# Performance work log

Hardware: AMD Instinct MI355X
Metric: run time of the kernel (lower is better)

The kernel has to match this reference:

```python
import jax, jax.numpy as jnp
import numpy as np

EMBED, ACT, DETER, STOCH, HID = 1536, 10, 2048, 64, 1024
T, B = 64, 256
LN_EPS = 1e-3


def _ln(x, s, b):
    mu = jnp.mean(x, axis=-1, keepdims=True)
    var = jnp.mean(jnp.square(x - mu), axis=-1, keepdims=True)
    return (x - mu) * jax.lax.rsqrt(var + LN_EPS) * s + b


def setup_inputs() -> dict:
    key = jax.random.key(0)
    ks = jax.random.split(key, 20)
    g = lambda k, shp, fan: jax.random.normal(k, shp, jnp.float32) * (1.0 / np.sqrt(fan))
    inp = {
        "embeds": jax.random.normal(ks[0], (T, B, EMBED), jnp.float32),
        "actions": jax.random.normal(ks[1], (T, B, ACT), jnp.float32),
        "h_t": jnp.zeros((B, DETER), jnp.float32),
        "z_t": jnp.zeros((B, STOCH), jnp.float32),
        "noise": jax.random.normal(ks[2], (T, B, STOCH), jnp.float32),
        # DeterNext
        "z_mlp_w": g(ks[3], (HID // 2, STOCH), STOCH),
        "z_mlp_b": jnp.zeros((HID // 2,), jnp.float32),
        "a_mlp_w": g(ks[4], (HID // 2, ACT), ACT),  # bias=False
        "ln_za_s": jnp.ones((HID,), jnp.float32),
        "ln_za_b": jnp.zeros((HID,), jnp.float32),
        # GRUCell (torch layout: [3*deter, in])
        "gru_wih": g(ks[5], (3 * DETER, HID), HID),
        "gru_whh": g(ks[6], (3 * DETER, DETER), DETER),
        "gru_bih": jnp.zeros((3 * DETER,), jnp.float32),
        "gru_bhh": jnp.zeros((3 * DETER,), jnp.float32),
        # PosteriorNext
        "post_h_w": g(ks[7], (HID, DETER), DETER),
        "post_h_b": jnp.zeros((HID,), jnp.float32),
        "post_e_w": g(ks[8], (HID, EMBED), EMBED),
        "post_e_b": jnp.zeros((HID,), jnp.float32),
        "ln_post_s": jnp.ones((HID,), jnp.float32),
        "ln_post_b": jnp.zeros((HID,), jnp.float32),
        "post_w": g(ks[9], (2 * STOCH, HID), HID),
        "post_b": jnp.zeros((2 * STOCH,), jnp.float32),
        # PriorNext
        "prior_h_w": g(ks[10], (HID, DETER), DETER),
        "prior_h_b": jnp.zeros((HID,), jnp.float32),
        "ln_prior_s": jnp.ones((HID,), jnp.float32),
        "ln_prior_b": jnp.zeros((HID,), jnp.float32),
        "prior_w": g(ks[11], (2 * STOCH, HID), HID),
        "prior_b": jnp.zeros((2 * STOCH,), jnp.float32),
    }
    return inp


def _rssm_forward(embeds, actions, h0, z0, noise,
                  z_mlp_w, z_mlp_b, a_mlp_w, ln_za_s, ln_za_b,
                  gru_wih, gru_whh, gru_bih, gru_bhh,
                  post_h_w, post_h_b, post_e_w, post_e_b, ln_post_s, ln_post_b,
                  post_w, post_b,
                  prior_h_w, prior_h_b, ln_prior_s, ln_prior_b, prior_w, prior_b):
    def step(carry, xs):
        h, z = carry
        e, a, n = xs
        # DeterNext: concat(z_mlp(z), a_mlp(a)) -> LN -> ELU
        x = jnp.concatenate([z @ z_mlp_w.T + z_mlp_b, a @ a_mlp_w.T], axis=-1)
        za = jax.nn.elu(_ln(x, ln_za_s, ln_za_b))
        # GRUCell
        gi = za @ gru_wih.T + gru_bih
        gh = h @ gru_whh.T + gru_bhh
        ir, iu, ic = jnp.split(gi, 3, axis=-1)
        hr, hu, hc = jnp.split(gh, 3, axis=-1)
        r = jax.nn.sigmoid(ir + hr)
        u = jax.nn.sigmoid(iu + hu)
        c = jnp.tanh(ic + r * hc)
        h1 = (1.0 - u) * c + u * h
        # PosteriorNext
        p = jax.nn.elu(_ln(h1 @ post_h_w.T + post_h_b + e @ post_e_w.T + post_e_b,
                           ln_post_s, ln_post_b))
        post = p @ post_w.T + post_b  # [B, 2*stoch]
        mean, sraw = jnp.split(post, 2, axis=-1)
        std = 2.0 * jax.nn.sigmoid(sraw) + 0.1
        z1 = mean + std * n  # rsample with externally-supplied noise
        return (h1, z1), (post, h1, z1)

    (_, _), (posts, states_h, post_z_samples) = jax.lax.scan(
        step, (h0, z0), (embeds, actions, noise))
    # batch prior over all timesteps
    pr = jax.nn.elu(_ln(states_h @ prior_h_w.T + prior_h_b, ln_prior_s, ln_prior_b))
    priors = pr @ prior_w.T + prior_b  # [T, B, 2*stoch]
    features = jnp.concatenate([states_h, post_z_samples], axis=-1)  # [T,B,deter+stoch]
    return priors, posts, post_z_samples, features


def reference(embeds, actions, h_t, z_t, noise,
              z_mlp_w, z_mlp_b, a_mlp_w, ln_za_s, ln_za_b,
              gru_wih, gru_whh, gru_bih, gru_bhh,
              post_h_w, post_h_b, post_e_w, post_e_b, ln_post_s, ln_post_b,
              post_w, post_b,
              prior_h_w, prior_h_b, ln_prior_s, ln_prior_b, prior_w, prior_b):
    return _rssm_forward(embeds, actions, h_t, z_t, noise,
                         z_mlp_w, z_mlp_b, a_mlp_w, ln_za_s, ln_za_b,
                         gru_wih, gru_whh, gru_bih, gru_bhh,
                         post_h_w, post_h_b, post_e_w, post_e_b, ln_post_s, ln_post_b,
                         post_w, post_b,
                         prior_h_w, prior_h_b, ln_prior_s, ln_prior_b, prior_w, prior_b)
```

## Files before the change

### kernel.cpp

```cpp
#include <hip/hip_runtime.h>

#define LN_EPS 1e-3f

typedef short s8v __attribute__((ext_vector_type(8)));
typedef float f4v __attribute__((ext_vector_type(4)));
typedef unsigned short u16;

#define MFMA16 __builtin_amdgcn_mfma_f32_16x16x32_bf16

__device__ __forceinline__ u16 f2bf(float f) {
  unsigned int x = __float_as_uint(f);
  x += 0x7fffu + ((x >> 16) & 1u);
  return (u16)(x >> 16);
}
__device__ __forceinline__ float bf2f(u16 u) {
  return __uint_as_float(((unsigned int)u) << 16);
}

__device__ __forceinline__ void glds16(const u16* g, void* l) {
  __builtin_amdgcn_global_load_lds(
      (const __attribute__((address_space(1))) void*)g,
      (__attribute__((address_space(3))) void*)l, 16, 0, 0);
}

#define RAW_BAR() do { __builtin_amdgcn_s_barrier(); __builtin_amdgcn_sched_barrier(0); } while (0)

__global__ void k_cvt(const float* __restrict__ src, u16* __restrict__ dst, int n) {
  int i = blockIdx.x * blockDim.x + threadIdx.x;
  int stride = gridDim.x * blockDim.x;
  for (; i < n; i += stride) dst[i] = f2bf(src[i]);
}

__global__ void k_packgru(const float* __restrict__ wih,
                          const float* __restrict__ whh, u16* __restrict__ wt) {
  int u = blockIdx.x * 256 + threadIdx.x;
  int nt = u / 73728;
  int r1 = u % 73728;
  int s = r1 / 1536;
  int r2 = r1 % 1536;
  int sub = r2 / 512;
  int r3 = r2 % 512;
  int ch = r3 / 64;
  int row = r3 % 64;
  int j = nt * 64 + row;
  int kbase = s * 64 + ch * 8;
  s8v v;
#pragma unroll
  for (int e = 0; e < 8; ++e) {
    int kk = kbase + e;
    float x;
    if (sub == 0) {
      x = kk < 1024 ? wih[(size_t)j * 1024 + kk] : whh[(size_t)j * 2048 + kk - 1024];
    } else if (sub == 1) {
// ... 56 lines not shown
  if (tid < 64) zsh[tid] = zsrc[b * 64 + tid];
  if (tid < 10) ash[tid] = act[b * 10 + tid];
  __syncthreads();
  float x[4];
#pragma unroll
  for (int i = 0; i < 2; ++i) {
    int c = tid + i * 256;
    const float4* wp = (const float4*)(zw + c * 64);
    float a = zb[c];
#pragma unroll
    for (int k = 0; k < 16; ++k) {
      float4 v = wp[k];
      a += zsh[k * 4] * v.x + zsh[k * 4 + 1] * v.y + zsh[k * 4 + 2] * v.z +
           zsh[k * 4 + 3] * v.w;
    }
    x[i] = a;
  }
#pragma unroll
  for (int i = 2; i < 4; ++i) {
    int c2 = tid + (i - 2) * 256;
    const float* wp = aw + c2 * 10;
    float a = 0.f;
#pragma unroll
    for (int k = 0; k < 10; ++k) a += ash[k] * wp[k];
    x[i] = a;
  }
  float s = x[0] + x[1] + x[2] + x[3];
#pragma unroll
  for (int o = 1; o < 64; o <<= 1) s += __shfl_xor(s, o);
  if ((tid & 63) == 0) wred[tid >> 6] = s;
  __syncthreads();
  float mu = (wred[0] + wred[1] + wred[2] + wred[3]) * (1.f / 1024.f);
  float q = 0.f;
#pragma unroll
  for (int i = 0; i < 4; ++i) {
    float d = x[i] - mu;
    q += d * d;
  }
#pragma unroll
  for (int o = 1; o < 64; o <<= 1) q += __shfl_xor(q, o);
  if ((tid & 63) == 0) wred[4 + (tid >> 6)] = q;
  __syncthreads();
  float rs = rsqrtf((wred[4] + wred[5] + wred[6] + wred[7]) * (1.f / 1024.f) + LN_EPS);
  int cols[4] = {tid, tid + 256, 512 + tid, 768 + tid};
#pragma unroll
  for (int i = 0; i < 4; ++i) {
    int c = cols[i];
    float y = (x[i] - mu) * rs * lns[c] + lnb[c];
    y = y > 0.f ? y : expm1f(y);
    za[(size_t)b * 1024 + c] = f2bf(y);
  }
}

__global__ __launch_bounds__(512) void k_gru(
    const u16* __restrict__ za, const u16* __restrict__ hcat_r,
    const u16* __restrict__ wt, const float* __restrict__ bih,
    const float* __restrict__ bhh, const float* __restrict__ hf_r,
    float* __restrict__ hf_w, u16* __restrict__ hcat_w,
    float* __restrict__ feat, int t) {
  const int hw = blockIdx.x;
  const int logical = (hw & 7) * 16 + (hw >> 3);
  const int mg = logical & 3;
  const int nt = logical >> 2;
  const int m0 = mg * 64;
  const int tid = threadIdx.x;
  const int lane = tid & 63;
  const int w = tid >> 6;
  const int lr = lane & 15, lk = lane >> 4;
  const int mh = w & 1, cq = w >> 1;

  __shared__ __align__(16) char bufs[3][32768];

  const int arow = w * 8 + (lane >> 3);
  const int acol8 = ((lane & 7) ^ (arow & 7)) * 8;
  const u16* aZ = za + (size_t)(m0 + arow) * 1024 + acol8;
  const u16* aH = hcat_r + (size_t)(m0 + arow) * 2048 + acol8;
  const u16* wtNt = wt + (size_t)nt * 48 * 12288;

  f4v accr0 = (f4v)(0.f), accr1 = (f4v)(0.f);
  f4v accu0 = (f4v)(0.f), accu1 = (f4v)(0.f);
  f4v acci0 = (f4v)(0.f), acci1 = (f4v)(0.f);
  f4v acch0 = (f4v)(0.f), acch1 = (f4v)(0.f);

#define G_STAGE(S) { \
    char* base = &bufs[(S) % 3][0]; \
    const u16* ap = ((S) < 16) ? (aZ + (S) * 64) : (aH + ((S) - 16) * 64); \
    glds16(ap, base + w * 1024); \
    const u16* bsrc = wtNt + (size_t)(S) * 12288; \
    _Pragma("unroll") for (int jj = 0; jj < 3; ++jj) { \
      int c = w + jj * 8; \
      glds16(bsrc + c * 512 + lane * 8, base + 8192 + c * 1024); \
    } }

#define G_COMP(S, X0, X1) { \
    char* base = &bufs[(S) % 3][0]; \
    _Pragma("unroll") for (int kk = 0; kk < 2; ++kk) { \
      int ch = kk * 4 + lk; \
      int r0 = mh * 32 + lr, r1 = mh * 32 + 16 + lr; \
      s8v a0 = *(const s8v*)(base + r0 * 128 + ((ch ^ (r0 & 7)) << 4)); \
      s8v a1 = *(const s8v*)(base + r1 * 128 + ((ch ^ (r1 & 7)) << 4)); \
      int boff = 8192 + ch * 1024 + ((cq * 16 + lr) << 4); \
      s8v br = *(const s8v*)(base + boff); \
      s8v bu = *(const s8v*)(base + boff + 8192); \
      s8v bx = *(const s8v*)(base + boff + 16384); \
      accr0 = MFMA16(a0, br, accr0, 0, 0, 0); \
      accr1 = MFMA16(a1, br, accr1, 0, 0, 0); \
      accu0 = MFMA16(a0, bu, accu0, 0, 0, 0); \
      accu1 = MFMA16(a1, bu, accu1, 0, 0, 0); \
      X0 = MFMA16(a0, bx, X0, 0, 0, 0); \
      X1 = MFMA16(a1, bx, X1, 0, 0, 0); \
    } }

  G_STAGE(0)
  G_STAGE(1)
  for (int s = 0; s < 48; ++s) {
    if (s + 2 < 48) { G_STAGE(s + 2) }
    if (s < 46) asm volatile("s_waitcnt vmcnt(8)" ::: "memory");
    else if (s == 46) asm volatile("s_waitcnt vmcnt(4)" ::: "memory");
    else asm volatile("s_waitcnt vmcnt(0)" ::: "memory");
    RAW_BAR();
    if (s < 16) { G_COMP(s, acci0, acci1) }
    else { G_COMP(s, acch0, acch1) }
    RAW_BAR();
  }
#undef G_STAGE
#undef G_COMP

  const int col = nt * 64 + cq * 16 + lr;
  const float b_r = bih[col] + bhh[col];
  const float b_u = bih[2048 + col] + bhh[2048 + col];
  const float b_ci = bih[4096 + col];
  const float b_ch = bhh[4096 + col];
#define G_EPI(AR, AU, AI, AH, MO) \
  _Pragma("unroll") for (int r = 0; r < 4; ++r) { \
    int grow = m0 + mh * 32 + (MO) + lk * 4 + r; \
    float vr = AR[r] + b_r; \
    float vu = AU[r] + b_u; \
    float ic = AI[r] + b_ci; \
    float hc = AH[r] + b_ch; \
    float rg = 1.f / (1.f + expf(-vr)); \
    float ug = 1.f / (1.f + expf(-vu)); \
    float c = tanhf(ic + rg * hc); \
    float hold = hf_r[(size_t)grow * 2048 + col]; \
    float h1 = (1.f - ug) * c + ug * hold; \
    hf_w[(size_t)grow * 2048 + col] = h1; \
    hcat_w[(size_t)grow * 2048 + col] = f2bf(h1); \
    feat[(size_t)(t * 256 + grow) * 2112 + col] = h1; \
  }
  G_EPI(accr0, accu0, acci0, acch0, 0)
  G_EPI(accr1, accu1, acci1, acch1, 16)
#undef G_EPI
}

__global__ __launch_bounds__(256) void k_post(
    const u16* __restrict__ hcat, const u16* __restrict__ wp,
    const float* __restrict__ bias, const u16* __restrict__ epart_t,
    float* __restrict__ xbuf) {
  const int hw = blockIdx.x;
  const int logical = (hw & 7) * 16 + (hw >> 3);
  const int mg = logical & 7, nt = logical >> 3;
  const int m0 = mg * 32;
  const int tid = threadIdx.x;
  const int lane = tid & 63;
  const int w = tid >> 6;
  const int lr = lane & 15, lk = lane >> 4;

  __shared__ __align__(16) char smem[2][12288];

  const int arow = 8 * w + (lane >> 3);
  const int acol8 = ((lane & 7) ^ (arow & 7)) * 8;
  const u16* aSrc = hcat + (size_t)(m0 + arow) * 2048 + acol8;
  const u16* wpNt = wp + (size_t)nt * 32 * 4096;

  f4v acc[2];
  acc[0] = (f4v)(0.f);
  acc[1] = (f4v)(0.f);

#define K2_STAGE(BB, S) { \
    char* base = &smem[BB][0]; \
    glds16(aSrc + (S) * 64, base + w * 1024); \
    const u16* bsrc = wpNt + (size_t)(S) * 4096; \
    _Pragma("unroll") for (int i = 0; i < 2; ++i) { \
      int cf = w + i * 4; \
      glds16(bsrc + (cf * 64 + lane) * 8, base + 4096 + cf * 1024); \
    } }

#define K2_COMP(BB) { \
    char* base = &smem[BB][0]; \
    _Pragma("unroll") for (int kk = 0; kk < 2; ++kk) { \
      int ch = kk * 4 + lk; \
      int r0 = lr, r1 = 16 + lr; \
      s8v a0 = *(const s8v*)(base + r0 * 128 + ((ch ^ (r0 & 7)) * 16)); \
      s8v a1 = *(const s8v*)(base + r1 * 128 + ((ch ^ (r1 & 7)) * 16)); \
      s8v b = *(const s8v*)(base + 4096 + ch * 1024 + (w * 16 + lr) * 16); \
      acc[0] = MFMA16(a0, b, acc[0], 0, 0, 0); \
      acc[1] = MFMA16(a1, b, acc[1], 0, 0, 0); \
    } }

  K2_STAGE(0, 0)
  for (int s = 0; s < 31; ++s) {
    K2_STAGE((s + 1) & 1, s + 1)
    asm volatile("s_waitcnt vmcnt(3)" ::: "memory");
    RAW_BAR();
    K2_COMP(s & 1)
    RAW_BAR();
  }
  {
    asm volatile("s_waitcnt vmcnt(0)" ::: "memory");
    RAW_BAR();
    K2_COMP(1)
  }
#undef K2_STAGE
#undef K2_COMP
  const int col = nt * 64 + w * 16 + lr;
#pragma unroll
  for (int m = 0; m < 2; ++m) {
#pragma unroll
    for (int r = 0; r < 4; ++r) {
      int grow = m0 + m * 16 + lk * 4 + r;
      float v = acc[m][r] + bias[col] + bf2f(epart_t[(size_t)grow * 1024 + col]);
      xbuf[(size_t)grow * 1024 + col] = v;
    }
  }
}

__global__ __launch_bounds__(512) void k_postz(
    const float* __restrict__ xb, const u16* __restrict__ pw,
    const float* __restrict__ lns, const float* __restrict__ lnb,
    const float* __restrict__ pb, float* __restrict__ posts_t,
    const float* __restrict__ noise_t, float* __restrict__ zout,
    float* __restrict__ feat, const u16* __restrict__ zwP,
    const float* __restrict__ zbv, const float* __restrict__ awT,
    const float* __restrict__ act_t, const float* __restrict__ lnzs,
    const float* __restrict__ lnzb, u16* __restrict__ za_out, int t) {
  const int m0 = blockIdx.x * 32;
  const int tid = threadIdx.x;
  const int lane = tid & 63;
  const int w = tid >> 6;
  const int lr = lane & 15, lk = lane >> 4;
  __shared__ __align__(16) u16 As[2][2048];
  __shared__ __align__(16) u16 Bs[2][8192];
  __shared__ float ps[32][132];
  __shared__ float lmu[32], lrsd[32];
  __shared__ __align__(16) u16 zbl[2048];
  __shared__ float ash[320];
  __shared__ __align__(16) char zal[65536];
  __shared__ float zmu[32], zrsd[32];
  __shared__ float psum[16][32], qsum[16][32];

  if (tid < 320) ash[tid] = act_t[m0 * 10 + tid];
  {
    int row = tid >> 4, sg = tid & 15;
    const float4* xp = (const float4*)(xb + (size_t)(m0 + row) * 1024 + sg * 64);
    float s = 0.f, q = 0.f;
#pragma unroll
    for (int i = 0; i < 16; ++i) {
      float4 v = xp[i];
      s += v.x + v.y + v.z + v.w;
      q += v.x * v.x + v.y * v.y + v.z * v.z + v.w * v.w;
    }
#pragma unroll
    for (int o = 1; o < 16; o <<= 1) {
      s += __shfl_xor(s, o);
      q += __shfl_xor(q, o);
    }
    if (sg == 0) {
      float mu = s * (1.f / 1024.f);
      lmu[row] = mu;
      lrsd[row] = rsqrtf(q * (1.f / 1024.f) - mu * mu + LN_EPS);
    }
  }
  __syncthreads();

#define K3_STAGEA(BB, S) if (tid < 256) { \
    int row = tid >> 3, k8 = tid & 7; \
    const float* xp = xb + (size_t)(m0 + row) * 1024 + (S) * 64 + k8 * 8; \
    float mu = lmu[row], rs = lrsd[row]; \
    s8v v; \
    _Pragma("unroll") for (int e = 0; e < 8; ++e) { \
      int c = (S) * 64 + k8 * 8 + e; \
      float y = (xp[e] - mu) * rs * lns[c] + lnb[c]; \
      y = y > 0.f ? y : expm1f(y); \
      v[e] = (short)f2bf(y); \
    } \
    *(s8v*)((char*)&As[BB][0] + row * 128 + ((k8 ^ (row & 7)) * 16)) = v; }

#define K3_STAGEB(BB, S) { \
    const u16* bsrc = pw + (size_t)(S) * 8192; \
    glds16(bsrc + (w * 2) * 512 + lane * 8, (char*)&Bs[BB][0] + w * 2048); \
    glds16(bsrc + (w * 2 + 1) * 512 + lane * 8, (char*)&Bs[BB][0] + w * 2048 + 1024); }

  f4v acc0 = (f4v)(0.f), acc1 = (f4v)(0.f);
  K3_STAGEA(0, 0)
  K3_STAGEB(0, 0)
  int buf = 0;
  for (int s = 0; s < 16; ++s) {
    if (s + 1 < 16) {
      K3_STAGEA(buf ^ 1, s + 1)
      K3_STAGEB(buf ^ 1, s + 1)
      asm volatile("s_waitcnt vmcnt(2) lgkmcnt(0)" ::: "memory");
    } else {
      asm volatile("s_waitcnt vmcnt(0) lgkmcnt(0)" ::: "memory");
    }
    RAW_BAR();
#pragma unroll
    for (int kk = 0; kk < 2; ++kk) {
      int ch = kk * 4 + lk;
      int r0 = lr, r1 = 16 + lr;
      s8v a0 = *(const s8v*)((char*)&As[buf][0] + r0 * 128 + ((ch ^ (r0 & 7)) * 16));
      s8v a1 = *(const s8v*)((char*)&As[buf][0] + r1 * 128 + ((ch ^ (r1 & 7)) * 16));
      s8v b = *(const s8v*)((char*)&Bs[buf][0] + ch * 2048 + (w * 16 + lr) * 16);
      acc0 = MFMA16(a0, b, acc0, 0, 0, 0);
      acc1 = MFMA16(a1, b, acc1, 0, 0, 0);
    }
    __builtin_amdgcn_s_barrier();
    buf ^= 1;
  }
#undef K3_STAGEA
#undef K3_STAGEB

  {
    int colp = w * 16 + lr;
#pragma unroll
    for (int r = 0; r < 4; ++r) {
      int row0 = lk * 4 + r;
      float v0 = acc0[r] + pb[colp];
      posts_t[(size_t)(m0 + row0) * 128 + colp] = v0;
      ps[row0][colp] = v0;
      float v1 = acc1[r] + pb[colp];
      posts_t[(size_t)(m0 + 16 + row0) * 128 + colp] = v1;
      ps[16 + row0][colp] = v1;
    }
  }
  __syncthreads();
#pragma unroll
  for (int q = 0; q < 4; ++q) {
    int e = q * 512 + tid;
    int row = e >> 6, j = e & 63;
    float mean = ps[row][j], sraw = ps[row][64 + j];
    float sd = 2.f / (1.f + expf(-sraw)) + 0.1f;
    float z = mean + sd * noise_t[(m0 + row) * 64 + j];
    zout[(m0 + row) * 64 + j] = z;
    feat[(size_t)(t * 256 + m0 + row) * 2112 + 2048 + j] = z;
    *(u16*)((char*)&zbl[0] + row * 128 + (((j >> 3) ^ (row & 7)) << 4) +
            (j & 7) * 2) = f2bf(z);
  }
  __syncthreads();

  {
    float acc[32];
#pragma unroll
    for (int r = 0; r < 32; ++r) acc[r] = 0.f;
#pragma unroll
    for (int k = 0; k < 10; ++k) {
      float wv = awT[k * 512 + tid];
#pragma unroll
      for (int r = 0; r < 32; ++r) acc[r] += ash[r * 10 + k] * wv;
    }
    int c = 512 + tid;
    int chs = c >> 3, cb = (c & 7) * 2;
#pragma unroll
    for (int r = 0; r < 32; ++r)
      *(u16*)(zal + r * 2048 + ((chs ^ (r & 7)) << 4) + cb) = f2bf(acc[r]);
  }
  for (int c4 = 0; c4 < 4; ++c4) {
    glds16(zwP + c4 * 8192 + (w * 2) * 512 + lane * 8, (char*)&Bs[0][0] + w * 2048);
    glds16(zwP + c4 * 8192 + (w * 2 + 1) * 512 + lane * 8,
           (char*)&Bs[0][0] + w * 2048 + 1024);
    asm volatile("s_waitcnt vmcnt(0)" ::: "memory");
    RAW_BAR();
    f4v z0 = (f4v)(0.f), z1 = (f4v)(0.f);
#pragma unroll
    for (int kk = 0; kk < 2; ++kk) {
      int ch = kk * 4 + lk;
      int r0 = lr, r1 = 16 + lr;
      s8v a0 = *(const s8v*)((char*)&zbl[0] + r0 * 128 + ((ch ^ (r0 & 7)) << 4));
      s8v a1 = *(const s8v*)((char*)&zbl[0] + r1 * 128 + ((ch ^ (r1 & 7)) << 4));
      s8v b = *(const s8v*)((char*)&Bs[0][0] + ch * 2048 + (w * 16 + lr) * 16);
      z0 = MFMA16(a0, b, z0, 0, 0, 0);
      z1 = MFMA16(a1, b, z1, 0, 0, 0);
    }
    int zcol = c4 * 128 + w * 16 + lr;
    int chz = zcol >> 3, cbz = (zcol & 7) * 2;
    float zbias = zbv[zcol];
#pragma unroll
    for (int r = 0; r < 4; ++r) {
      int ra = lk * 4 + r, rb = 16 + lk * 4 + r;
      *(u16*)(zal + ra * 2048 + ((chz ^ (ra & 7)) << 4) + cbz) = f2bf(z0[r] + zbias);
      *(u16*)(zal + rb * 2048 + ((chz ^ (rb & 7)) << 4) + cbz) = f2bf(z1[r] + zbias);
    }
    RAW_BAR();
  }
  __syncthreads();
  {
    int row = tid & 31, g = tid >> 5;
    float s = 0.f, q = 0.f;
#pragma unroll
    for (int jj = 0; jj < 8; ++jj) {
      int chunk = g * 8 + jj;
      s8v v = *(const s8v*)(zal + row * 2048 + ((chunk ^ (row & 7)) << 4));
#pragma unroll
      for (int e = 0; e < 8; ++e) {
        float x = bf2f((u16)v[e]);
        s += x;
        q += x * x;
      }
    }
    psum[g][row] = s;
    qsum[g][row] = q;
    __syncthreads();
    if (tid < 32) {
      float ss = 0.f, qq = 0.f;
#pragma unroll
      for (int gg = 0; gg < 16; ++gg) {
        ss += psum[gg][tid];
        qq += qsum[gg][tid];
      }
      float mu = ss * (1.f / 1024.f);
      zmu[tid] = mu;
      zrsd[tid] = rsqrtf(qq * (1.f / 1024.f) - mu * mu + LN_EPS);
    }
  }
  __syncthreads();
  {
    int row = tid >> 4, g = tid & 15;
    float mu = zmu[row], rs = zrsd[row];
    u16* dst = za_out + (size_t)(m0 + row) * 1024 + g * 64;
#pragma unroll
    for (int jj = 0; jj < 8; ++jj) {
      int chunk = g * 8 + jj;
      s8v v = *(const s8v*)(zal + row * 2048 + ((chunk ^ (row & 7)) << 4));
      s8v o;
#pragma unroll
      for (int e = 0; e < 8; ++e) {
        int c = chunk * 8 + e;
        float y = (bf2f((u16)v[e]) - mu) * rs * lnzs[c] + lnzb[c];
        y = y > 0.f ? y : expm1f(y);
        o[e] = (short)f2bf(y);
      }
      *(s8v*)(dst + jj * 8) = o;
    }
  }
}

template <bool AF32, bool OUTBF16>
__global__ __launch_bounds__(512) void k_gemm8(
    const void* __restrict__ Av, int lda, const u16* __restrict__ Bw, int ldb,
    int nstage, float* __restrict__ Cf, u16* __restrict__ Cb, int ldc,
    const float* __restrict__ bias) {
  const int bx = blockIdx.x, by = blockIdx.y;
  const int tid = threadIdx.x;
  const int m0 = bx * 64;
  const int n0 = by * 128;
  __shared__ __align__(16) u16 As[64][72];
  __shared__ __align__(16) u16 Bs[128][72];
  const int lane = tid & 63;
  const int w = tid >> 6;
  const int wr = w >> 2;
  const int wc = w & 3;
  const int lr = lane & 15;
  const int lk = lane >> 4;

  f4v acc[2][2];
#pragma unroll
  for (int m = 0; m < 2; ++m)
#pragma unroll
    for (int n = 0; n < 2; ++n) acc[m][n] = (f4v)(0.0f);

  for (int s = 0; s < nstage; ++s) {
    const int k0 = s << 6;
    {
      int row = tid >> 3, k8 = (tid & 7) << 3;
      if (AF32) {
        const float* ap = (const float*)Av + (size_t)(m0 + row) * lda + k0 + k8;
        float4 f0 = *(const float4*)ap;
        float4 f1 = *(const float4*)(ap + 4);
        s8v v;
        v[0] = (short)f2bf(f0.x); v[1] = (short)f2bf(f0.y);
        v[2] = (short)f2bf(f0.z); v[3] = (short)f2bf(f0.w);
        v[4] = (short)f2bf(f1.x); v[5] = (short)f2bf(f1.y);
        v[6] = (short)f2bf(f1.z); v[7] = (short)f2bf(f1.w);
        *(s8v*)&As[row][k8] = v;
      } else {
        *(s8v*)&As[row][k8] =
            *(const s8v*)((const u16*)Av + (size_t)(m0 + row) * lda + k0 + k8);
      }
    }
#pragma unroll
    for (int it = 0; it < 2; ++it) {
      int c = tid + it * 512;
      int row = c >> 3, k8 = (c & 7) << 3;
      *(s8v*)&Bs[row][k8] = *(const s8v*)(Bw + (size_t)(n0 + row) * ldb + k0 + k8);
    }
    __syncthreads();
// ... 90 lines not shown
  const float* ln_za_b = (const float*)d_in[9];
  const float* gru_wih = (const float*)d_in[10];
  const float* gru_whh = (const float*)d_in[11];
  const float* gru_bih = (const float*)d_in[12];
  const float* gru_bhh = (const float*)d_in[13];
  const float* post_h_w = (const float*)d_in[14];
  const float* post_h_b = (const float*)d_in[15];
  const float* post_e_w = (const float*)d_in[16];
  const float* post_e_b = (const float*)d_in[17];
  const float* ln_post_s = (const float*)d_in[18];
  const float* ln_post_b = (const float*)d_in[19];
  const float* post_w = (const float*)d_in[20];
  const float* post_b = (const float*)d_in[21];
  const float* prior_h_w = (const float*)d_in[22];
  const float* prior_h_b = (const float*)d_in[23];
  const float* ln_prior_s = (const float*)d_in[24];
  const float* ln_prior_b = (const float*)d_in[25];
  const float* prior_w = (const float*)d_in[26];
  const float* prior_b = (const float*)d_in[27];

  float* out = (float*)d_out;
  float* out_priors = out;
  float* out_posts = out + 2097152;
  float* out_z = out + 4194304;
  float* out_feat = out + 5242880;

  char* ws = (char*)d_ws;
  size_t off = 0;
  auto alloc = [&](size_t bytes) {
    char* p = ws + off;
    off += (bytes + 255) & ~(size_t)255;
    return p;
  };
  char* regW = alloc((size_t)32 * 48 * 12288 * 2);
  u16* wt = (u16*)regW;
  u16* prx_b = (u16*)regW;
  u16* posthP = (u16*)alloc((size_t)1024 * 2048 * 2);
  u16* postwP = (u16*)alloc((size_t)128 * 1024 * 2);
  u16* poste_b = (u16*)alloc((size_t)1024 * 1536 * 2);
  u16* priorh_b = (u16*)alloc((size_t)1024 * 2048 * 2);
  u16* priorw_b = (u16*)alloc((size_t)128 * 1024 * 2);
  u16* zwP = (u16*)alloc((size_t)512 * 64 * 2);
  float* awT = (float*)alloc((size_t)10 * 512 * 4);
  u16* hcat0 = (u16*)alloc((size_t)256 * 2048 * 2);
  u16* hcat1 = (u16*)alloc((size_t)256 * 2048 * 2);
  float* hf0 = (float*)alloc((size_t)256 * 2048 * 4);
  float* hf1 = (float*)alloc((size_t)256 * 2048 * 4);
  float* xbuf = (float*)alloc((size_t)256 * 1024 * 4);
  u16* za = (u16*)alloc((size_t)256 * 1024 * 2);
  char* regU = alloc((size_t)16384 * 1024 * 2);
  u16* e_part = (u16*)regU;
  u16* p_pr = (u16*)regU;

  u16* hcat[2] = {hcat0, hcat1};
  float* hf[2] = {hf0, hf1};

  k_packgru<<<9216, 256, 0, stream>>>(gru_wih, gru_whh, wt);
  k_packB<<<1024, 256, 0, stream>>>(post_h_w, posthP, 2048, 64, 262144);
  k_packB<<<64, 256, 0, stream>>>(post_w, postwP, 1024, 128, 16384);
  k_packB<<<16, 256, 0, stream>>>(z_mlp_w, zwP, 64, 128, 4096);
  k_trA<<<20, 256, 0, stream>>>(a_mlp_w, awT);
  k_cvt<<<512, 256, 0, stream>>>(post_e_w, poste_b, 1024 * 1536);
  k_cvt<<<512, 256, 0, stream>>>(prior_h_w, priorh_b, 1024 * 2048);
  k_cvt<<<64, 256, 0, stream>>>(prior_w, priorw_b, 128 * 1024);
  k_hinit<<<2048, 256, 0, stream>>>(h_t, hf0, hcat0);
  k_za0<<<256, 256, 0, stream>>>(z_t, actions, z_mlp_w, z_mlp_b, a_mlp_w,
                                 ln_za_s, ln_za_b, za);

  k_gemm8<true, true><<<dim3(256, 8), 512, 0, stream>>>(
      embeds, 1536, poste_b, 1536, 24, nullptr, e_part, 1024, post_e_b);

  for (int t = 0; t < 64; ++t) {
    const int rI = t & 1, wI = rI ^ 1;
    k_gru<<<128, 512, 0, stream>>>(za, hcat[rI], wt, gru_bih, gru_bhh, hf[rI],
                                   hf[wI], hcat[wI], out_feat, t);
    k_post<<<128, 256, 0, stream>>>(hcat[wI], posthP, post_h_b,
                                    e_part + (size_t)t * 262144, xbuf);
    k_postz<<<8, 512, 0, stream>>>(
        xbuf, postwP, ln_post_s, ln_post_b, post_b,
        out_posts + (size_t)t * 32768, noise + (size_t)t * 16384,
        out_z + (size_t)t * 16384, out_feat, zwP, z_mlp_b, awT,
        actions + (size_t)(t + 1 < 64 ? t + 1 : t) * 2560, ln_za_s, ln_za_b,
        za, t);
  }

  k_gemm8<true, true><<<dim3(256, 8), 512, 0, stream>>>(
      out_feat, 2112, priorh_b, 2048, 32, nullptr, prx_b, 1024, prior_h_b);
  k_lnelu<<<16384, 256, 0, stream>>>(prx_b, ln_prior_s, ln_prior_b, p_pr);
  k_gemm8<false, false><<<dim3(256, 1), 512, 0, stream>>>(
      p_pr, 1024, priorw_b, 1024, 16, out_priors, nullptr, 128, prior_b);
}
```

Before: 8.619 ms.

## Fuse per-timestep GRU/posterior kernels into one persistent cooperative scan kernel

```diff
diff --git a/kernel.cpp b/kernel.cpp
--- a/kernel.cpp
+++ b/kernel.cpp
@@ -1,4 +1,7 @@
 #include <hip/hip_runtime.h>
+#include <hip/hip_cooperative_groups.h>
+
+namespace cg = cooperative_groups;
 
 #define LN_EPS 1e-3f
 
@@ -161,38 +164,72 @@
   }
 }
 
-__global__ __launch_bounds__(512) void k_gru(
-    const u16* __restrict__ za, const u16* __restrict__ hcat_r,
-    const u16* __restrict__ wt, const float* __restrict__ bih,
-    const float* __restrict__ bhh, const float* __restrict__ hf_r,
-    float* __restrict__ hf_w, u16* __restrict__ hcat_w,
-    float* __restrict__ feat, int t) {
-  const int hw = blockIdx.x;
-  const int logical = (hw & 7) * 16 + (hw >> 3);
-  const int mg = logical & 3;
-  const int nt = logical >> 2;
-  const int m0 = mg * 64;
+struct ScanArgs {
+  const u16* wt;
+  const float* bih;
+  const float* bhh;
+  u16* hcat0;
+  u16* hcat1;
+  float* hf0;
+  float* hf1;
+  u16* za;
+  const u16* posthP;
+  const float* post_h_b;
+  const u16* e_part;
+  float* xbuf;
+  const u16* postwP;
+  const float* ln_post_s;
+  const float* ln_post_b;
+  const float* post_b;
+  float* out_posts;
+  const float* noise;
+  float* out_z;
+  float* out_feat;
+  const u16* zwP;
+  const float* z_mlp_b;
+  const float* awT;
+  const float* actions;
+  const float* ln_za_s;
+  const float* ln_za_b;
+};
+
+__global__ __launch_bounds__(512) void k_scan(ScanArgs a) {
+  cg::grid_group grid = cg::this_grid();
+  const int bid = blockIdx.x;
   const int tid = threadIdx.x;
   const int lane = tid & 63;
   const int w = tid >> 6;
   const int lr = lane & 15, lk = lane >> 4;
-  const int mh = w & 1, cq = w >> 1;
-
-  __shared__ __align__(16) char bufs[3][32768];
-
-  const int arow = w * 8 + (lane >> 3);
-  const int acol8 = ((lane & 7) ^ (arow & 7)) * 8;
-  const u16* aZ = za + (size_t)(m0 + arow) * 1024 + acol8;
-  const u16* aH = hcat_r + (size_t)(m0 + arow) * 2048 + acol8;
-  const u16* wtNt = wt + (size_t)nt * 48 * 12288;
-
-  f4v accr0 = (f4v)(0.f), accr1 = (f4v)(0.f);
-  f4v accu0 = (f4v)(0.f), accu1 = (f4v)(0.f);
-  f4v acci0 = (f4v)(0.f), acci1 = (f4v)(0.f);
-  f4v acch0 = (f4v)(0.f), acch1 = (f4v)(0.f);
+
+  __shared__ __align__(16) char sm[133376];
+
+  for (int t = 0; t < 64; ++t) {
+    const int rI = t & 1;
+    const u16* hcat_r = rI ? a.hcat1 : a.hcat0;
+    u16* hcat_w = rI ? a.hcat0 : a.hcat1;
+    const float* hf_r = rI ? a.hf1 : a.hf0;
+    float* hf_w = rI ? a.hf0 : a.hf1;
+
+    {
+      const int logical = (bid & 7) * 16 + (bid >> 3);
+      const int mg = logical & 3;
+      const int nt = logical >> 2;
+      const int m0 = mg * 64;
+      const int mh = w & 1, cq = w >> 1;
+
+      const int arow = w * 8 + (lane >> 3);
+      const int acol8 = ((lane & 7) ^ (arow & 7)) * 8;
+      const u16* aZ = a.za + (size_t)(m0 + arow) * 1024 + acol8;
+      const u16* aH = hcat_r + (size_t)(m0 + arow) * 2048 + acol8;
+      const u16* wtNt = a.wt + (size_t)nt * 48 * 12288;
+
+      f4v accr0 = (f4v)(0.f), accr1 = (f4v)(0.f);
+      f4v accu0 = (f4v)(0.f), accu1 = (f4v)(0.f);
+      f4v acci0 = (f4v)(0.f), acci1 = (f4v)(0.f);
+      f4v acch0 = (f4v)(0.f), acch1 = (f4v)(0.f);
 
 #define G_STAGE(S) { \
-    char* base = &bufs[(S) % 3][0]; \
+    char* base = sm + ((S) % 3) * 32768; \
     const u16* ap = ((S) < 16) ? (aZ + (S) * 64) : (aH + ((S) - 16) * 64); \
     glds16(ap, base + w * 1024); \
     const u16* bsrc = wtNt + (size_t)(S) * 12288; \
@@ -202,7 +239,7 @@
     } }
 
 #define G_COMP(S, X0, X1) { \
-    char* base = &bufs[(S) % 3][0]; \
+    char* base = sm + ((S) % 3) * 32768; \
     _Pragma("unroll") for (int kk = 0; kk < 2; ++kk) { \
       int ch = kk * 4 + lk; \
       int r0 = mh * 32 + lr, r1 = mh * 32 + 16 + lr; \
@@ -220,26 +257,26 @@
       X1 = MFMA16(a1, bx, X1, 0, 0, 0); \
     } }
 
-  G_STAGE(0)
-  G_STAGE(1)
-  for (int s = 0; s < 48; ++s) {
-    if (s + 2 < 48) { G_STAGE(s + 2) }
-    if (s < 46) asm volatile("s_waitcnt vmcnt(8)" ::: "memory");
-    else if (s == 46) asm volatile("s_waitcnt vmcnt(4)" ::: "memory");
-    else asm volatile("s_waitcnt vmcnt(0)" ::: "memory");
-    RAW_BAR();
-    if (s < 16) { G_COMP(s, acci0, acci1) }
-    else { G_COMP(s, acch0, acch1) }
-    RAW_BAR();
-  }
+      G_STAGE(0)
+      G_STAGE(1)
+      for (int s = 0; s < 48; ++s) {
+        if (s + 2 < 48) { G_STAGE(s + 2) }
+        if (s < 46) asm volatile("s_waitcnt vmcnt(8)" ::: "memory");
+        else if (s == 46) asm volatile("s_waitcnt vmcnt(4)" ::: "memory");
+        else asm volatile("s_waitcnt vmcnt(0)" ::: "memory");
+        RAW_BAR();
+        if (s < 16) { G_COMP(s, acci0, acci1) }
+        else { G_COMP(s, acch0, acch1) }
+        RAW_BAR();
+      }
 #undef G_STAGE
 #undef G_COMP
 
-  const int col = nt * 64 + cq * 16 + lr;
-  const float b_r = bih[col] + bhh[col];
-  const float b_u = bih[2048 + col] + bhh[2048 + col];
-  const float b_ci = bih[4096 + col];
-  const float b_ch = bhh[4096 + col];
+      const int col = nt * 64 + cq * 16 + lr;
+      const float b_r = a.bih[col] + a.bhh[col];
+      const float b_u = a.bih[2048 + col] + a.bhh[2048 + col];
+      const float b_ci = a.bih[4096 + col];
+      const float b_ch = a.bhh[4096 + col];
 #define G_EPI(AR, AU, AI, AH, MO) \
   _Pragma("unroll") for (int r = 0; r < 4; ++r) { \
     int grow = m0 + mh * 32 + (MO) + lk * 4 + r; \
@@ -254,301 +291,287 @@
     float h1 = (1.f - ug) * c + ug * hold; \
     hf_w[(size_t)grow * 2048 + col] = h1; \
     hcat_w[(size_t)grow * 2048 + col] = f2bf(h1); \
-    feat[(size_t)(t * 256 + grow) * 2112 + col] = h1; \
-  }
-  G_EPI(accr0, accu0, acci0, acch0, 0)
-  G_EPI(accr1, accu1, acci1, acch1, 16)
+    a.out_feat[(size_t)(t * 256 + grow) * 2112 + col] = h1; \
+  }
+      G_EPI(accr0, accu0, acci0, acch0, 0)
+      G_EPI(accr1, accu1, acci1, acch1, 16)
 #undef G_EPI
-}
-
-__global__ __launch_bounds__(256) void k_post(
-    const u16* __restrict__ hcat, const u16* __restrict__ wp,
-    const float* __restrict__ bias, const u16* __restrict__ epart_t,
-    float* __restrict__ xbuf) {
-  const int hw = blockIdx.x;
-  const int logical = (hw & 7) * 16 + (hw >> 3);
-  const int mg = logical & 7, nt = logical >> 3;
-  const int m0 = mg * 32;
-  const int tid = threadIdx.x;
-  const int lane = tid & 63;
-  const int w = tid >> 6;
-  const int lr = lane & 15, lk = lane >> 4;
-
-  __shared__ __align__(16) char smem[2][12288];
-
-  const int arow = 8 * w + (lane >> 3);
-  const int acol8 = ((lane & 7) ^ (arow & 7)) * 8;
-  const u16* aSrc = hcat + (size_t)(m0 + arow) * 2048 + acol8;
-  const u16* wpNt = wp + (size_t)nt * 32 * 4096;
-
-  f4v acc[2];
-  acc[0] = (f4v)(0.f);
-  acc[1] = (f4v)(0.f);
-
-#define K2_STAGE(BB, S) { \
-    char* base = &smem[BB][0]; \
-    glds16(aSrc + (S) * 64, base + w * 1024); \
-    const u16* bsrc = wpNt + (size_t)(S) * 4096; \
-    _Pragma("unroll") for (int i = 0; i < 2; ++i) { \
-      int cf = w + i * 4; \
-      glds16(bsrc + (cf * 64 + lane) * 8, base + 4096 + cf * 1024); \
-    } }
-
-#define K2_COMP(BB) { \
-    char* base = &smem[BB][0]; \
+    }
+    grid.sync();
+
+    {
+      const int logical = (bid & 7) * 16 + (bid >> 3);
+      const int mg = logical & 7, nt = logical >> 3;
+      const int m0 = mg * 32;
+      const int mh = w & 1, cq = w >> 1;
+
+      const int arow = 8 * w + (lane >> 3);
+      const int acol8 = ((lane & 7) ^ (arow & 7)) * 8;
+      const u16* aSrc = hcat_w + (size_t)(m0 + arow) * 2048 + acol8;
+      const u16* wpNt = a.posthP + (size_t)nt * 32 * 4096;
+      const u16* epart_t = a.e_part + (size_t)t * 262144;
+
+      f4v acc = (f4v)(0.f);
+
+#define P_STAGE(BB, S) { \
+    char* base = sm + (BB) * 12288; \
+    if (w < 4) glds16(aSrc + (S) * 64, base + w * 1024); \
+    glds16(wpNt + (size_t)(S) * 4096 + (w * 64 + lane) * 8, base + 4096 + w * 1024); }
+
+#define P_COMP(BB) { \
+    char* base = sm + (BB) * 12288; \
     _Pragma("unroll") for (int kk = 0; kk < 2; ++kk) { \
       int ch = kk * 4 + lk; \
-      int r0 = lr, r1 = 16 + lr; \
-      s8v a0 = *(const s8v*)(base + r0 * 128 + ((ch ^ (r0 & 7)) * 16)); \
-      s8v a1 = *(const s8v*)(base + r1 * 128 + ((ch ^ (r1 & 7)) * 16)); \
-      s8v b = *(const s8v*)(base + 4096 + ch * 1024 + (w * 16 + lr) * 16); \
-      acc[0] = MFMA16(a0, b, acc[0], 0, 0, 0); \
-      acc[1] = MFMA16(a1, b, acc[1], 0, 0, 0); \
+      int r = mh * 16 + lr; \
+      s8v av = *(const s8v*)(base + r * 128 + ((ch ^ (r & 7)) << 4)); \
+      s8v bv = *(const s8v*)(base + 4096 + ch * 1024 + ((cq * 16 + lr) << 4)); \
+      acc = MFMA16(av, bv, acc, 0, 0, 0); \
     } }
 
-  K2_STAGE(0, 0)
-  for (int s = 0; s < 31; ++s) {
-    K2_STAGE((s + 1) & 1, s + 1)
-    asm volatile("s_waitcnt vmcnt(3)" ::: "memory");
-    RAW_BAR();
-    K2_COMP(s & 1)
-    RAW_BAR();
-  }
-  {
-    asm volatile("s_waitcnt vmcnt(0)" ::: "memory");
-    RAW_BAR();
-    K2_COMP(1)
-  }
-#undef K2_STAGE
-#undef K2_COMP
-  const int col = nt * 64 + w * 16 + lr;
-#pragma unroll
-  for (int m = 0; m < 2; ++m) {
-#pragma unroll
-    for (int r = 0; r < 4; ++r) {
-      int grow = m0 + m * 16 + lk * 4 + r;
-      float v = acc[m][r] + bias[col] + bf2f(epart_t[(size_t)grow * 1024 + col]);
-      xbuf[(size_t)grow * 1024 + col] = v;
+      P_STAGE(0, 0)
+      for (int s = 0; s < 31; ++s) {
+        P_STAGE((s + 1) & 1, s + 1)
+        if (w < 4) { asm volatile("s_waitcnt vmcnt(2)" ::: "memory"); }
+        else { asm volatile("s_waitcnt vmcnt(1)" ::: "memory"); }
+        RAW_BAR();
+        P_COMP(s & 1)
+        RAW_BAR();
+      }
+      {
+        asm volatile("s_waitcnt vmcnt(0)" ::: "memory");
+        RAW_BAR();
+        P_COMP(1)
+      }
+#undef P_STAGE
+#undef P_COMP
+      const int col = nt * 64 + cq * 16 + lr;
+#pragma unroll
+      for (int r = 0; r < 4; ++r) {
+        int grow = m0 + mh * 16 + lk * 4 + r;
+        float v = acc[r] + a.post_h_b[col] + bf2f(epart_t[(size_t)grow * 1024 + col]);
+        a.xbuf[(size_t)grow * 1024 + col] = v;
+      }
     }
-  }
-}
-
-__global__ __launch_bounds__(512) void k_postz(
-    const float* __restrict__ xb, const u16* __restrict__ pw,
-    const float* __restrict__ lns, const float* __restrict__ lnb,
-    const float* __restrict__ pb, float* __restrict__ posts_t,
-    const float* __restrict__ noise_t, float* __restrict__ zout,
-    float* __restrict__ feat, const u16* __restrict__ zwP,
-    const float* __restrict__ zbv, const float* __restrict__ awT,
-    const float* __restrict__ act_t, const float* __restrict__ lnzs,
-    const float* __restrict__ lnzb, u16* __restrict__ za_out, int t) {
-  const int m0 = blockIdx.x * 32;
-  const int tid = threadIdx.x;
-  const int lane = tid & 63;
-  const int w = tid >> 6;
-  const int lr = lane & 15, lk = lane >> 4;
-  __shared__ __align__(16) u16 As[2][2048];
-  __shared__ __align__(16) u16 Bs[2][8192];
-  __shared__ float ps[32][132];
-  __shared__ float lmu[32], lrsd[32];
-  __shared__ __align__(16) u16 zbl[2048];
-  __shared__ float ash[320];
-  __shared__ __align__(16) char zal[65536];
-  __shared__ float zmu[32], zrsd[32];
-  __shared__ float psum[16][32], qsum[16][32];
-
-  if (tid < 320) ash[tid] = act_t[m0 * 10 + tid];
-  {
-    int row = tid >> 4, sg = tid & 15;
-    const float4* xp = (const float4*)(xb + (size_t)(m0 + row) * 1024 + sg * 64);
-    float s = 0.f, q = 0.f;
-#pragma unroll
-    for (int i = 0; i < 16; ++i) {
-      float4 v = xp[i];
-      s += v.x + v.y + v.z + v.w;
-      q += v.x * v.x + v.y * v.y + v.z * v.z + v.w * v.w;
-    }
-#pragma unroll
-    for (int o = 1; o < 16; o <<= 1) {
-      s += __shfl_xor(s, o);
-      q += __shfl_xor(q, o);
-    }
-    if (sg == 0) {
-      float mu = s * (1.f / 1024.f);
-      lmu[row] = mu;
-      lrsd[row] = rsqrtf(q * (1.f / 1024.f) - mu * mu + LN_EPS);
-    }
-  }
-  __syncthreads();
-
-#define K3_STAGEA(BB, S) if (tid < 256) { \
+    grid.sync();
+
+    if (bid < 8) {
+      const int m0 = bid * 32;
+      float* posts_t = a.out_posts + (size_t)t * 32768;
+      const float* noise_t = a.noise + (size_t)t * 16384;
+      float* zout = a.out_z + (size_t)t * 16384;
+      const float* act_t = a.actions + (size_t)(t + 1 < 64 ? t + 1 : t) * 2560;
+      const float* xb = a.xbuf;
+
+      char* AsB = sm;
+      char* BsB = sm + 8192;
+      float* ps = (float*)(sm + 40960);
+      float* lmu = (float*)(sm + 57856);
+      float* lrsd = (float*)(sm + 57984);
+      char* zblB = sm + 58112;
+      float* ash = (float*)(sm + 62208);
+      char* zal = sm + 63488;
+      float* zmu = (float*)(sm + 129024);
+      float* zrsd = (float*)(sm + 129152);
+      float* psum = (float*)(sm + 129280);
+      float* qsum = (float*)(sm + 131328);
+
+      if (tid < 320) ash[tid] = act_t[m0 * 10 + tid];
+      {
+        int row = tid >> 4, sg = tid & 15;
+        const float4* xp = (const float4*)(xb + (size_t)(m0 + row) * 1024 + sg * 64);
+        float s = 0.f, q = 0.f;
+#pragma unroll
+        for (int i = 0; i < 16; ++i) {
+          float4 v = xp[i];
+          s += v.x + v.y + v.z + v.w;
+          q += v.x * v.x + v.y * v.y + v.z * v.z + v.w * v.w;
+        }
+#pragma unroll
+        for (int o = 1; o < 16; o <<= 1) {
+          s += __shfl_xor(s, o);
+          q += __shfl_xor(q, o);
+        }
+        if (sg == 0) {
+          float mu = s * (1.f / 1024.f);
+          lmu[row] = mu;
+          lrsd[row] = rsqrtf(q * (1.f / 1024.f) - mu * mu + LN_EPS);
+        }
+      }
+      __syncthreads();
+
+#define Z_STAGEA(BB, S) if (tid < 256) { \
     int row = tid >> 3, k8 = tid & 7; \
     const float* xp = xb + (size_t)(m0 + row) * 1024 + (S) * 64 + k8 * 8; \
     float mu = lmu[row], rs = lrsd[row]; \
     s8v v; \
     _Pragma("unroll") for (int e = 0; e < 8; ++e) { \
       int c = (S) * 64 + k8 * 8 + e; \
-      float y = (xp[e] - mu) * rs * lns[c] + lnb[c]; \
+      float y = (xp[e] - mu) * rs * a.ln_post_s[c] + a.ln_post_b[c]; \
       y = y > 0.f ? y : expm1f(y); \
       v[e] = (short)f2bf(y); \
     } \
-    *(s8v*)((char*)&As[BB][0] + row * 128 + ((k8 ^ (row & 7)) * 16)) = v; }
-
-#define K3_STAGEB(BB, S) { \
-    const u16* bsrc = pw + (size_t)(S) * 8192; \
-    glds16(bsrc + (w * 2) * 512 + lane * 8, (char*)&Bs[BB][0] + w * 2048); \
-    glds16(bsrc + (w * 2 + 1) * 512 + lane * 8, (char*)&Bs[BB][0] + w * 2048 + 1024); }
-
-  f4v acc0 = (f4v)(0.f), acc1 = (f4v)(0.f);
-  K3_STAGEA(0, 0)
-  K3_STAGEB(0, 0)
-  int buf = 0;
-  for (int s = 0; s < 16; ++s) {
-    if (s + 1 < 16) {
-      K3_STAGEA(buf ^ 1, s + 1)
-      K3_STAGEB(buf ^ 1, s + 1)
-      asm volatile("s_waitcnt vmcnt(2) lgkmcnt(0)" ::: "memory");
-    } else {
-      asm volatile("s_waitcnt vmcnt(0) lgkmcnt(0)" ::: "memory");
+    *(s8v*)(AsB + (BB) * 4096 + row * 128 + ((k8 ^ (row & 7)) * 16)) = v; }
+
+#define Z_STAGEB(BB, S) { \
+    const u16* bsrc = a.postwP + (size_t)(S) * 8192; \
+    glds16(bsrc + (w * 2) * 512 + lane * 8, BsB + (BB) * 16384 + w * 2048); \
+    glds16(bsrc + (w * 2 + 1) * 512 + lane * 8, BsB + (BB) * 16384 + w * 2048 + 1024); }
+
+      f4v acc0 = (f4v)(0.f), acc1 = (f4v)(0.f);
+      Z_STAGEA(0, 0)
+      Z_STAGEB(0, 0)
+      int buf = 0;
+      for (int s = 0; s < 16; ++s) {
+        if (s + 1 < 16) {
+          Z_STAGEA(buf ^ 1, s + 1)
+          Z_STAGEB(buf ^ 1, s + 1)
+          asm volatile("s_waitcnt vmcnt(2) lgkmcnt(0)" ::: "memory");
+        } else {
+          asm volatile("s_waitcnt vmcnt(0) lgkmcnt(0)" ::: "memory");
+        }
+        RAW_BAR();
+#pragma unroll
+        for (int kk = 0; kk < 2; ++kk) {
+          int ch = kk * 4 + lk;
+          int r0 = lr, r1 = 16 + lr;
+          s8v a0 = *(const s8v*)(AsB + buf * 4096 + r0 * 128 + ((ch ^ (r0 & 7)) * 16));
+          s8v a1 = *(const s8v*)(AsB + buf * 4096 + r1 * 128 + ((ch ^ (r1 & 7)) * 16));
+          s8v b = *(const s8v*)(BsB + buf * 16384 + ch * 2048 + (w * 16 + lr) * 16);
+          acc0 = MFMA16(a0, b, acc0, 0, 0, 0);
+          acc1 = MFMA16(a1, b, acc1, 0, 0, 0);
+        }
+        __builtin_amdgcn_s_barrier();
+        buf ^= 1;
+      }
+#undef Z_STAGEA
+#undef Z_STAGEB
+
+      {
+        int colp = w * 16 + lr;
+#pragma unroll
+        for (int r = 0; r < 4; ++r) {
+          int row0 = lk * 4 + r;
+          float v0 = acc0[r] + a.post_b[colp];
+          posts_t[(size_t)(m0 + row0) * 128 + colp] = v0;
+          ps[row0 * 132 + colp] = v0;
+          float v1 = acc1[r] + a.post_b[colp];
+          posts_t[(size_t)(m0 + 16 + row0) * 128 + colp] = v1;
+          ps[(16 + row0) * 132 + colp] = v1;
+        }
+      }
+      __syncthreads();
+#pragma unroll
+      for (int q = 0; q < 4; ++q) {
+        int e = q * 512 + tid;
+        int row = e >> 6, j = e & 63;
+        float mean = ps[row * 132 + j], sraw = ps[row * 132 + 64 + j];
+        float sd = 2.f / (1.f + expf(-sraw)) + 0.1f;
+        float z = mean + sd * noise_t[(m0 + row) * 64 + j];
+        zout[(m0 + row) * 64 + j] = z;
+        a.out_feat[(size_t)(t * 256 + m0 + row) * 2112 + 2048 + j] = z;
+        *(u16*)(zblB + row * 128 + (((j >> 3) ^ (row & 7)) << 4) + (j & 7) * 2) =
+            f2bf(z);
+      }
+      __syncthreads();
+
+      {
+        float accv[32];
+#pragma unroll
+        for (int r = 0; r < 32; ++r) accv[r] = 0.f;
+#pragma unroll
+        for (int k = 0; k < 10; ++k) {
+          float wv = a.awT[k * 512 + tid];
+#pragma unroll
+          for (int r = 0; r < 32; ++r) accv[r] += ash[r * 10 + k] * wv;
+        }
+        int c = 512 + tid;
+        int chs = c >> 3, cb = (c & 7) * 2;
+#pragma unroll
+        for (int r = 0; r < 32; ++r)
+          *(u16*)(zal + r * 2048 + ((chs ^ (r & 7)) << 4) + cb) = f2bf(accv[r]);
+      }
+      for (int c4 = 0; c4 < 4; ++c4) {
+        glds16(a.zwP + c4 * 8192 + (w * 2) * 512 + lane * 8, BsB + w * 2048);
+        glds16(a.zwP + c4 * 8192 + (w * 2 + 1) * 512 + lane * 8,
+               BsB + w * 2048 + 1024);
+        asm volatile("s_waitcnt vmcnt(0)" ::: "memory");
+        RAW_BAR();
+        f4v z0 = (f4v)(0.f), z1 = (f4v)(0.f);
+#pragma unroll
+        for (int kk = 0; kk < 2; ++kk) {
+          int ch = kk * 4 + lk;
+          int r0 = lr, r1 = 16 + lr;
+          s8v a0 = *(const s8v*)(zblB + r0 * 128 + ((ch ^ (r0 & 7)) << 4));
+          s8v a1 = *(const s8v*)(zblB + r1 * 128 + ((ch ^ (r1 & 7)) << 4));
+          s8v b = *(const s8v*)(BsB + ch * 2048 + (w * 16 + lr) * 16);
+          z0 = MFMA16(a0, b, z0, 0, 0, 0);
+          z1 = MFMA16(a1, b, z1, 0, 0, 0);
+        }
+        int zcol = c4 * 128 + w * 16 + lr;
+        int chz = zcol >> 3, cbz = (zcol & 7) * 2;
+        float zbias = a.z_mlp_b[zcol];
+#pragma unroll
+        for (int r = 0; r < 4; ++r) {
+          int ra = lk * 4 + r, rb = 16 + lk * 4 + r;
+          *(u16*)(zal + ra * 2048 + ((chz ^ (ra & 7)) << 4) + cbz) =
+              f2bf(z0[r] + zbias);
+          *(u16*)(zal + rb * 2048 + ((chz ^ (rb & 7)) << 4) + cbz) =
+              f2bf(z1[r] + zbias);
+        }
+        RAW_BAR();
+      }
+      __syncthreads();
+      {
+        int row = tid & 31, g = tid >> 5;
+        float s = 0.f, q = 0.f;
+#pragma unroll
+        for (int jj = 0; jj < 8; ++jj) {
+          int chunk = g * 8 + jj;
+          s8v v = *(const s8v*)(zal + row * 2048 + ((chunk ^ (row & 7)) << 4));
+#pragma unroll
+          for (int e = 0; e < 8; ++e) {
+            float x = bf2f((u16)v[e]);
+            s += x;
+            q += x * x;
+          }
+        }
+        psum[g * 32 + row] = s;
+        qsum[g * 32 + row] = q;
+        __syncthreads();
+        if (tid < 32) {
+          float ss = 0.f, qq = 0.f;
+#pragma unroll
+          for (int gg = 0; gg < 16; ++gg) {
+            ss += psum[gg * 32 + tid];
+            qq += qsum[gg * 32 + tid];
+          }
+          float mu = ss * (1.f / 1024.f);
+          zmu[tid] = mu;
+          zrsd[tid] = rsqrtf(qq * (1.f / 1024.f) - mu * mu + LN_EPS);
+        }
+      }
+      __syncthreads();
+      {
+        int row = tid >> 4, g = tid & 15;
+        float mu = zmu[row], rs = zrsd[row];
+        u16* dst = a.za + (size_t)(m0 + row) * 1024 + g * 64;
+#pragma unroll
+        for (int jj = 0; jj < 8; ++jj) {
+          int chunk = g * 8 + jj;
+          s8v v = *(const s8v*)(zal + row * 2048 + ((chunk ^ (row & 7)) << 4));
+          s8v o;
+#pragma unroll
+          for (int e = 0; e < 8; ++e) {
+            int c = chunk * 8 + e;
+            float y = (bf2f((u16)v[e]) - mu) * rs * a.ln_za_s[c] + a.ln_za_b[c];
+            y = y > 0.f ? y : expm1f(y);
+            o[e] = (short)f2bf(y);
+          }
+          *(s8v*)(dst + jj * 8) = o;
+        }
+      }
     }
-    RAW_BAR();
-#pragma unroll
-    for (int kk = 0; kk < 2; ++kk) {
-      int ch = kk * 4 + lk;
-      int r0 = lr, r1 = 16 + lr;
-      s8v a0 = *(const s8v*)((char*)&As[buf][0] + r0 * 128 + ((ch ^ (r0 & 7)) * 16));
-      s8v a1 = *(const s8v*)((char*)&As[buf][0] + r1 * 128 + ((ch ^ (r1 & 7)) * 16));
-      s8v b = *(const s8v*)((char*)&Bs[buf][0] + ch * 2048 + (w * 16 + lr) * 16);
-      acc0 = MFMA16(a0, b, acc0, 0, 0, 0);
-      acc1 = MFMA16(a1, b, acc1, 0, 0, 0);
-    }
-    __builtin_amdgcn_s_barrier();
-    buf ^= 1;
-  }
-#undef K3_STAGEA
-#undef K3_STAGEB
-
-  {
-    int colp = w * 16 + lr;
-#pragma unroll
-    for (int r = 0; r < 4; ++r) {
-      int row0 = lk * 4 + r;
-      float v0 = acc0[r] + pb[colp];
-      posts_t[(size_t)(m0 + row0) * 128 + colp] = v0;
-      ps[row0][colp] = v0;
-      float v1 = acc1[r] + pb[colp];
-      posts_t[(size_t)(m0 + 16 + row0) * 128 + colp] = v1;
-      ps[16 + row0][colp] = v1;
-    }
-  }
-  __syncthreads();
-#pragma unroll
-  for (int q = 0; q < 4; ++q) {
-    int e = q * 512 + tid;
-    int row = e >> 6, j = e & 63;
-    float mean = ps[row][j], sraw = ps[row][64 + j];
-    float sd = 2.f / (1.f + expf(-sraw)) + 0.1f;
-    float z = mean + sd * noise_t[(m0 + row) * 64 + j];
-    zout[(m0 + row) * 64 + j] = z;
-    feat[(size_t)(t * 256 + m0 + row) * 2112 + 2048 + j] = z;
-    *(u16*)((char*)&zbl[0] + row * 128 + (((j >> 3) ^ (row & 7)) << 4) +
-            (j & 7) * 2) = f2bf(z);
-  }
-  __syncthreads();
-
-  {
-    float acc[32];
-#pragma unroll
-    for (int r = 0; r < 32; ++r) acc[r] = 0.f;
-#pragma unroll
-    for (int k = 0; k < 10; ++k) {
-      float wv = awT[k * 512 + tid];
-#pragma unroll
-      for (int r = 0; r < 32; ++r) acc[r] += ash[r * 10 + k] * wv;
-    }
-    int c = 512 + tid;
-    int chs = c >> 3, cb = (c & 7) * 2;
-#pragma unroll
-    for (int r = 0; r < 32; ++r)
-      *(u16*)(zal + r * 2048 + ((chs ^ (r & 7)) << 4) + cb) = f2bf(acc[r]);
-  }
-  for (int c4 = 0; c4 < 4; ++c4) {
-    glds16(zwP + c4 * 8192 + (w * 2) * 512 + lane * 8, (char*)&Bs[0][0] + w * 2048);
-    glds16(zwP + c4 * 8192 + (w * 2 + 1) * 512 + lane * 8,
-           (char*)&Bs[0][0] + w * 2048 + 1024);
-    asm volatile("s_waitcnt vmcnt(0)" ::: "memory");
-    RAW_BAR();
-    f4v z0 = (f4v)(0.f), z1 = (f4v)(0.f);
-#pragma unroll
-    for (int kk = 0; kk < 2; ++kk) {
-      int ch = kk * 4 + lk;
-      int r0 = lr, r1 = 16 + lr;
-      s8v a0 = *(const s8v*)((char*)&zbl[0] + r0 * 128 + ((ch ^ (r0 & 7)) << 4));
-      s8v a1 = *(const s8v*)((char*)&zbl[0] + r1 * 128 + ((ch ^ (r1 & 7)) << 4));
-      s8v b = *(const s8v*)((char*)&Bs[0][0] + ch * 2048 + (w * 16 + lr) * 16);
-      z0 = MFMA16(a0, b, z0, 0, 0, 0);
-      z1 = MFMA16(a1, b, z1, 0, 0, 0);
-    }
-    int zcol = c4 * 128 + w * 16 + lr;
-    int chz = zcol >> 3, cbz = (zcol & 7) * 2;
-    float zbias = zbv[zcol];
-#pragma unroll
-    for (int r = 0; r < 4; ++r) {
-      int ra = lk * 4 + r, rb = 16 + lk * 4 + r;
-      *(u16*)(zal + ra * 2048 + ((chz ^ (ra & 7)) << 4) + cbz) = f2bf(z0[r] + zbias);
-      *(u16*)(zal + rb * 2048 + ((chz ^ (rb & 7)) << 4) + cbz) = f2bf(z1[r] + zbias);
-    }
-    RAW_BAR();
-  }
-  __syncthreads();
-  {
-    int row = tid & 31, g = tid >> 5;
-    float s = 0.f, q = 0.f;
-#pragma unroll
-    for (int jj = 0; jj < 8; ++jj) {
-      int chunk = g * 8 + jj;
-      s8v v = *(const s8v*)(zal + row * 2048 + ((chunk ^ (row & 7)) << 4));
-#pragma unroll
-      for (int e = 0; e < 8; ++e) {
-        float x = bf2f((u16)v[e]);
-        s += x;
-        q += x * x;
-      }
-    }
-    psum[g][row] = s;
-    qsum[g][row] = q;
-    __syncthreads();
-    if (tid < 32) {
-      float ss = 0.f, qq = 0.f;
-#pragma unroll
-      for (int gg = 0; gg < 16; ++gg) {
-        ss += psum[gg][tid];
-        qq += qsum[gg][tid];
-      }
-      float mu = ss * (1.f / 1024.f);
-      zmu[tid] = mu;
-      zrsd[tid] = rsqrtf(qq * (1.f / 1024.f) - mu * mu + LN_EPS);
-    }
-  }
-  __syncthreads();
-  {
-    int row = tid >> 4, g = tid & 15;
-    float mu = zmu[row], rs = zrsd[row];
-    u16* dst = za_out + (size_t)(m0 + row) * 1024 + g * 64;
-#pragma unroll
-    for (int jj = 0; jj < 8; ++jj) {
-      int chunk = g * 8 + jj;
-      s8v v = *(const s8v*)(zal + row * 2048 + ((chunk ^ (row & 7)) << 4));
-      s8v o;
-#pragma unroll
-      for (int e = 0; e < 8; ++e) {
-        int c = chunk * 8 + e;
-        float y = (bf2f((u16)v[e]) - mu) * rs * lnzs[c] + lnzb[c];
-        y = y > 0.f ? y : expm1f(y);
-        o[e] = (short)f2bf(y);
-      }
-      *(s8v*)(dst + jj * 8) = o;
-    }
+    grid.sync();
   }
 }
 
@@ -745,9 +768,6 @@
   u16* e_part = (u16*)regU;
   u16* p_pr = (u16*)regU;
 
-  u16* hcat[2] = {hcat0, hcat1};
-  float* hf[2] = {hf0, hf1};
-
   k_packgru<<<9216, 256, 0, stream>>>(gru_wih, gru_whh, wt);
   k_packB<<<1024, 256, 0, stream>>>(post_h_w, posthP, 2048, 64, 262144);
   k_packB<<<64, 256, 0, stream>>>(post_w, postwP, 1024, 128, 16384);
@@ -763,19 +783,36 @@
   k_gemm8<true, true><<<dim3(256, 8), 512, 0, stream>>>(
       embeds, 1536, poste_b, 1536, 24, nullptr, e_part, 1024, post_e_b);
 
-  for (int t = 0; t < 64; ++t) {
-    const int rI = t & 1, wI = rI ^ 1;
-    k_gru<<<128, 512, 0, stream>>>(za, hcat[rI], wt, gru_bih, gru_bhh, hf[rI],
-                                   hf[wI], hcat[wI], out_feat, t);
-    k_post<<<128, 256, 0, stream>>>(hcat[wI], posthP, post_h_b,
-                                    e_part + (size_t)t * 262144, xbuf);
-    k_postz<<<8, 512, 0, stream>>>(
-        xbuf, postwP, ln_post_s, ln_post_b, post_b,
-        out_posts + (size_t)t * 32768, noise + (size_t)t * 16384,
-        out_z + (size_t)t * 16384, out_feat, zwP, z_mlp_b, awT,
-        actions + (size_t)(t + 1 < 64 ? t + 1 : t) * 2560, ln_za_s, ln_za_b,
-        za, t);
-  }
+  ScanArgs sa;
+  sa.wt = wt;
+  sa.bih = gru_bih;
+  sa.bhh = gru_bhh;
+  sa.hcat0 = hcat0;
+  sa.hcat1 = hcat1;
+  sa.hf0 = hf0;
+  sa.hf1 = hf1;
+  sa.za = za;
+  sa.posthP = posthP;
+  sa.post_h_b = post_h_b;
+  sa.e_part = e_part;
+  sa.xbuf = xbuf;
+  sa.postwP = postwP;
+  sa.ln_post_s = ln_post_s;
+  sa.ln_post_b = ln_post_b;
+  sa.post_b = post_b;
+  sa.out_posts = out_posts;
+  sa.noise = noise;
+  sa.out_z = out_z;
+  sa.out_feat = out_feat;
+  sa.zwP = zwP;
+  sa.z_mlp_b = z_mlp_b;
+  sa.awT = awT;
+  sa.actions = actions;
+  sa.ln_za_s = ln_za_s;
+  sa.ln_za_b = ln_za_b;
+  void* kargs[] = {(void*)&sa};
+  hipLaunchCooperativeKernel((const void*)k_scan, dim3(128), dim3(512), kargs,
+                             0, stream);
 
   k_gemm8<true, true><<<dim3(256, 8), 512, 0, stream>>>(
       out_feat, 2112, priorh_b, 2048, 32, nullptr, prx_b, 1024, prior_h_b);
```

Measured after the change: 14.02 ms. 1.63x slower.
